# Kernel optimization log

Hardware: AMD Instinct MI355X
Metric: run time of the kernel (lower is better)

## Reference

```python
import jax, jax.numpy as jnp
import numpy as np

INPUT_DIM = 1024
EMBED_DIM = 1024
NUM_HEADS = 16
HEAD_DIM = EMBED_DIM // NUM_HEADS


def _xavier_uniform(key, shape):
    fan_in, fan_out = shape[1], shape[0]
    limit = float(np.sqrt(6.0 / (fan_in + fan_out)))
    return jax.random.uniform(key, shape, jnp.float32, -limit, limit)


def setup_inputs() -> dict:
    key = jax.random.key(0)
    kx, kqkv, ko = jax.random.split(key, 3)
    x = jax.random.normal(kx, (2, 2048, INPUT_DIM), jnp.float32)
    # torch Linear stores weight as [out, in]; we keep that convention
    w_qkv = _xavier_uniform(kqkv, (3 * EMBED_DIM, INPUT_DIM))
    b_qkv = jnp.zeros((3 * EMBED_DIM,), jnp.float32)
    w_o = _xavier_uniform(ko, (EMBED_DIM, EMBED_DIM))
    b_o = jnp.zeros((EMBED_DIM,), jnp.float32)
    return {"x": x, "w_qkv": w_qkv, "b_qkv": b_qkv, "w_o": w_o, "b_o": b_o}


def reference(x, w_qkv, b_qkv, w_o, b_o):
    B, S, _ = x.shape
    H, D = NUM_HEADS, HEAD_DIM
    qkv = jnp.einsum("bsi,oi->bso", x, w_qkv) + b_qkv          # [B,S,3E]
    qkv = qkv.reshape(B, S, H, 3 * D).transpose(0, 2, 1, 3)    # [B,H,S,3D]
    q, k, v = jnp.split(qkv, 3, axis=-1)                        # each [B,H,S,D]
    scores = jnp.einsum("bhqd,bhkd->bhqk", q, k) / jnp.sqrt(jnp.float32(D))
    attn = jax.nn.softmax(scores, axis=-1)                      # [B,H,S,S]
    vals = jnp.einsum("bhqk,bhkd->bhqd", attn, v)               # [B,H,S,D]
    vals = vals.transpose(0, 2, 1, 3).reshape(B, S, H * D)      # [B,S,E]
    return jnp.einsum("bse,oe->bso", vals, w_o) + b_o
```

## Files before the change

kernel.cpp:

```cpp
#include <hip/hip_runtime.h>
#include <hip/hip_bf16.h>


typedef __attribute__((ext_vector_type(8))) short bf16x8;
typedef __attribute__((ext_vector_type(4))) short bf16x4;
typedef __attribute__((ext_vector_type(4))) float f32x4;

#define MFMA16(a, b, c) __builtin_amdgcn_mfma_f32_16x16x32_bf16((a), (b), (c), 0, 0, 0)

#if __has_builtin(__builtin_amdgcn_exp2f)
#define EXP2F(x) __builtin_amdgcn_exp2f(x)
#else
#define EXP2F(x) exp2f(x)
#endif

static __device__ __forceinline__ unsigned short f2bf_bits(float v) {
    __hip_bfloat16 h = __float2bfloat16(v);
    return *reinterpret_cast<unsigned short*>(&h);
}

static __device__ __forceinline__ bf16x8 cvt8(const float* p) {
    const f32x4 a = reinterpret_cast<const f32x4*>(p)[0];
    const f32x4 b = reinterpret_cast<const f32x4*>(p)[1];
    bf16x8 r;
    r[0] = (short)f2bf_bits(a[0]); r[1] = (short)f2bf_bits(a[1]);
    r[2] = (short)f2bf_bits(a[2]); r[3] = (short)f2bf_bits(a[3]);
    r[4] = (short)f2bf_bits(b[0]); r[5] = (short)f2bf_bits(b[1]);
    r[6] = (short)f2bf_bits(b[2]); r[7] = (short)f2bf_bits(b[3]);
    return r;
}

__device__ __forceinline__ bf16x8 ldg8(const __hip_bfloat16* p) {
    return *reinterpret_cast<const bf16x8*>(p);
}

__device__ __forceinline__ void load16_lds(const __hip_bfloat16* g, unsigned short* l) {
    __builtin_amdgcn_global_load_lds(
        (const __attribute__((address_space(1))) void*)g,
        (__attribute__((address_space(3))) void*)l, 16, 0, 0);
}

__global__ __launch_bounds__(256)
void cast2_f32_bf16(const float* __restrict__ x, __hip_bfloat16* __restrict__ xb,
                    const float* __restrict__ w, __hip_bfloat16* __restrict__ wb) {
    const int bid = blockIdx.x;
    const float* src = (bid < 512) ? x : w;
    __hip_bfloat16* dst = (bid < 512) ? xb : wb;
    const int rb = (bid < 512) ? bid : (bid - 512);
    const size_t base = (size_t)rb * 8192 + (size_t)threadIdx.x * 32;
#pragma unroll
    for (int i = 0; i < 4; ++i)
        *reinterpret_cast<bf16x8*>(dst + base + i * 8) = cvt8(src + base + i * 8);
}

__global__ __launch_bounds__(256)
void cast_f32_bf16(const float* __restrict__ src, __hip_bfloat16* __restrict__ dst) {
    const size_t base = ((size_t)blockIdx.x * 256 + threadIdx.x) * 32;
#pragma unroll
    for (int i = 0; i < 4; ++i)
        *reinterpret_cast<bf16x8*>(dst + base + i * 8) = cvt8(src + base + i * 8);
}

__global__ __launch_bounds__(256)
void qkv_gemm(const __hip_bfloat16* __restrict__ xb,
              const __hip_bfloat16* __restrict__ wb,
              const float* __restrict__ bqkv,
              __hip_bfloat16* __restrict__ Q,
              __hip_bfloat16* __restrict__ K,
              __hip_bfloat16* __restrict__ Vt) {
    __shared__ unsigned short As[128 * 32];
    __shared__ unsigned short Bs[128 * 32];

    const int tid  = threadIdx.x;
    const int lane = tid & 63;
    const int wv   = tid >> 6;
    const int quad = lane >> 4;
    const int l16  = lane & 15;
    const int wm   = wv >> 1;
    const int wn   = wv & 1;

    const int bid = blockIdx.x;
    const int xcd = bid & 7;
    const int r   = bid >> 3;
    const int m0  = (r / 3) * 128;
    const int n0  = (xcd * 3 + (r % 3)) * 128;

    const __hip_bfloat16* agl = xb + (size_t)(m0 + wv * 32 + (lane >> 2)) * 1024 + (lane & 3) * 8;
    const __hip_bfloat16* bgl = wb + (size_t)(n0 + wv * 32 + (lane >> 2)) * 1024 + (lane & 3) * 8;
    unsigned short* al0 = &As[(wv * 32) * 32];
    unsigned short* al1 = &As[(wv * 32 + 16) * 32];
    unsigned short* bl0 = &Bs[(wv * 32) * 32];
    unsigned short* bl1 = &Bs[(wv * 32 + 16) * 32];

    f32x4 zv = {0.f, 0.f, 0.f, 0.f};
    f32x4 acc[4][4];
#pragma unroll
    for (int ii = 0; ii < 4; ++ii)
#pragma unroll
        for (int jj = 0; jj < 4; ++jj) acc[ii][jj] = zv;

    for (int k0 = 0; k0 < 1024; k0 += 32) {
        load16_lds(agl + k0, al0);
        load16_lds(agl + 16 * 1024 + k0, al1);
        load16_lds(bgl + k0, bl0);
        load16_lds(bgl + 16 * 1024 + k0, bl1);
        __syncthreads();
        bf16x8 af[4], bf[4];
#pragma unroll
        for (int ii = 0; ii < 4; ++ii)
            af[ii] = *reinterpret_cast<const bf16x8*>(
                &As[(wm * 64 + ii * 16 + l16) * 32 + quad * 8]);
#pragma unroll
        for (int jj = 0; jj < 4; ++jj)
            bf[jj] = *reinterpret_cast<const bf16x8*>(
                &Bs[(wn * 64 + jj * 16 + l16) * 32 + quad * 8]);
#pragma unroll
        for (int ii = 0; ii < 4; ++ii)
#pragma unroll
            for (int jj = 0; jj < 4; ++jj)
                acc[ii][jj] = MFMA16(af[ii], bf[jj], acc[ii][jj]);
        __syncthreads();
    }

    const float QSCALE = 0.18033688011f;

#pragma unroll
    for (int jj = 0; jj < 4; ++jj) {
        const int n = n0 + wn * 64 + jj * 16 + l16;
        const float bias = bqkv[n];
        const int h = n / 192;
        const int r2 = n - h * 192;
        const int t = r2 >> 6;
        const int d = r2 & 63;
#pragma unroll
        for (int ii = 0; ii < 4; ++ii) {
#pragma unroll
            for (int i = 0; i < 4; ++i) {
                const int m = m0 + wm * 64 + ii * 16 + quad * 4 + i;
                const int b = m >> 11;
                const int s = m & 2047;
                const int bh = b * 16 + h;
                float v = acc[ii][jj][i] + bias;
                if (t == 0) {
                    Q[((size_t)bh * 2048 + s) * 64 + d] = __float2bfloat16(v * QSCALE);
                } else if (t == 1) {
                    K[((size_t)bh * 2048 + s) * 64 + d] = __float2bfloat16(v);
                } else {
                    Vt[((size_t)bh * 64 + d) * 2048 + s] = __float2bfloat16(v);
                }
            }
        }
    }
}

__global__ __launch_bounds__(256)
void attn_kernel(const __hip_bfloat16* __restrict__ Q,
                 const __hip_bfloat16* __restrict__ K,
                 const __hip_bfloat16* __restrict__ Vt,
                 __hip_bfloat16* __restrict__ AO) {
    __shared__ unsigned short Ks0[32 * 40];
    __shared__ unsigned short Ks1[32 * 40];
    __shared__ unsigned short Vs[64 * 40];

    const int tid  = threadIdx.x;
    const int lane = tid & 63;
    const int wv   = tid >> 6;
    const int quad = lane >> 4;
    const int l16  = lane & 15;

    const int blk = blockIdx.x;
    const int xcd = blk & 7;
    const int sub = blk >> 3;
    const int bh  = xcd * 4 + (sub & 3);
    const int qb  = sub >> 2;
    const int q0  = qb * 128 + wv * 32;
    const int b   = bh >> 4;
    const int h   = bh & 15;

    const __hip_bfloat16* Qp = Q  + (size_t)bh * 131072;
    const __hip_bfloat16* Kp = K  + (size_t)bh * 131072;
    const __hip_bfloat16* Vp = Vt + (size_t)bh * 131072;

    bf16x8 bQ[2][2];
#pragma unroll
    for (int t = 0; t < 2; ++t)
#pragma unroll
        for (int dh = 0; dh < 2; ++dh)
            bQ[t][dh] = ldg8(Qp + (size_t)(q0 + t * 16 + l16) * 64 + dh * 32 + quad * 8);

    const int kr = tid >> 3;
    const int kc = (tid & 7) * 8;
    const int kb = kr & 7;
    const int sig = (kb < 4) ? ((kr >> 3) * 4 + kb) : (16 + (kr >> 3) * 4 + (kb - 4));
    unsigned short* kw = (kc < 32) ? &Ks0[sig * 40 + kc] : &Ks1[sig * 40 + (kc - 32)];
    const int vr = tid >> 2;
    const int vc = (tid & 3) * 8;
    unsigned short* vw = &Vs[vr * 40 + vc];

    f32x4 zv = {0.f, 0.f, 0.f, 0.f};
    f32x4 Of[2][4];
#pragma unroll
    for (int t = 0; t < 2; ++t)
#pragma unroll
        for (int jj = 0; jj < 4; ++jj) Of[t][jj] = zv;
    float li[2] = {0.f, 0.f};

    for (int kt = 0; kt < 64; ++kt) {
        const int key0 = kt * 32;

        const bf16x8 gk = ldg8(Kp + (size_t)(key0 + kr) * 64 + kc);
        const bf16x8 gv = ldg8(Vp + (size_t)vr * 2048 + key0 + vc);
        __syncthreads();
        *reinterpret_cast<bf16x8*>(kw) = gk;
        *reinterpret_cast<bf16x8*>(vw) = gv;
        __syncthreads();

        const bf16x8 aKA0 = *reinterpret_cast<const bf16x8*>(&Ks0[l16 * 40 + quad * 8]);
        const bf16x8 aKA1 = *reinterpret_cast<const bf16x8*>(&Ks1[l16 * 40 + quad * 8]);
        const bf16x8 aKB0 = *reinterpret_cast<const bf16x8*>(&Ks0[(16 + l16) * 40 + quad * 8]);
        const bf16x8 aKB1 = *reinterpret_cast<const bf16x8*>(&Ks1[(16 + l16) * 40 + quad * 8]);
        bf16x8 aV[4];
#pragma unroll
        for (int jj = 0; jj < 4; ++jj)
            aV[jj] = *reinterpret_cast<const bf16x8*>(&Vs[(jj * 16 + l16) * 40 + quad * 8]);

        f32x4 sA[2], sB[2];
#pragma unroll
        for (int t = 0; t < 2; ++t) {
            sA[t] = zv; sB[t] = zv;
            sA[t] = MFMA16(aKA0, bQ[t][0], sA[t]);
            sA[t] = MFMA16(aKA1, bQ[t][1], sA[t]);
            sB[t] = MFMA16(aKB0, bQ[t][0], sB[t]);
            sB[t] = MFMA16(aKB1, bQ[t][1], sB[t]);
        }

#pragma unroll
        for (int t = 0; t < 2; ++t) {
            float pA[4], pB[4];
#pragma unroll
            for (int i = 0; i < 4; ++i) {
                pA[i] = EXP2F(sA[t][i]);
                pB[i] = EXP2F(sB[t][i]);
            }
            li[t] += ((pA[0] + pA[1]) + (pA[2] + pA[3]))
                   + ((pB[0] + pB[1]) + (pB[2] + pB[3]));

            bf16x8 bP;
            bP[0] = (short)f2bf_bits(pA[0]); bP[1] = (short)f2bf_bits(pA[1]);
            bP[2] = (short)f2bf_bits(pA[2]); bP[3] = (short)f2bf_bits(pA[3]);
            bP[4] = (short)f2bf_bits(pB[0]); bP[5] = (short)f2bf_bits(pB[1]);
            bP[6] = (short)f2bf_bits(pB[2]); bP[7] = (short)f2bf_bits(pB[3]);

#pragma unroll
            for (int jj = 0; jj < 4; ++jj)
                Of[t][jj] = MFMA16(aV[jj], bP, Of[t][jj]);
        }
    }

#pragma unroll
    for (int t = 0; t < 2; ++t) {
        li[t] += __shfl_xor(li[t], 16);
        li[t] += __shfl_xor(li[t], 32);
    }

#pragma unroll
    for (int t = 0; t < 2; ++t) {
        const float linv = 1.f / li[t];
        const int s = q0 + t * 16 + l16;
        __hip_bfloat16* aop = AO + (((size_t)b * 2048 + s) * 16 + h) * 64;
#pragma unroll
        for (int jj = 0; jj < 4; ++jj) {
            bf16x4 pk;
#pragma unroll
            for (int i = 0; i < 4; ++i)
                pk[i] = (short)f2bf_bits(Of[t][jj][i] * linv);
            *reinterpret_cast<bf16x4*>(aop + jj * 16 + quad * 4) = pk;
        }
    }
}

__global__ __launch_bounds__(256)
void out_gemm(const __hip_bfloat16* __restrict__ A,
              const __hip_bfloat16* __restrict__ wob,
              const float* __restrict__ bo,
              float* __restrict__ out) {
    __shared__ unsigned short As[64 * 32];
    __shared__ unsigned short Bs[128 * 32];

    const int tid  = threadIdx.x;
    const int lane = tid & 63;
    const int wv   = tid >> 6;
    const int quad = lane >> 4;
    const int l16  = lane & 15;
    const int wm   = wv >> 1;
    const int wn   = wv & 1;

    const int bid = blockIdx.x;
    const int m0  = (bid >> 3) * 64;
    const int n0  = (bid & 7) * 128;

    const __hip_bfloat16* agl = A   + (size_t)(m0 + wv * 16 + (lane >> 2)) * 1024 + (lane & 3) * 8;
    const __hip_bfloat16* bgl = wob + (size_t)(n0 + wv * 32 + (lane >> 2)) * 1024 + (lane & 3) * 8;
    unsigned short* al0 = &As[(wv * 16) * 32];
    unsigned short* bl0 = &Bs[(wv * 32) * 32];
    unsigned short* bl1 = &Bs[(wv * 32 + 16) * 32];

    f32x4 zv = {0.f, 0.f, 0.f, 0.f};
    f32x4 acc[2][4];
#pragma unroll
    for (int ii = 0; ii < 2; ++ii)
#pragma unroll
        for (int jj = 0; jj < 4; ++jj) acc[ii][jj] = zv;

    for (int k0 = 0; k0 < 1024; k0 += 32) {
        load16_lds(agl + k0, al0);
        load16_lds(bgl + k0, bl0);
        load16_lds(bgl + 16 * 1024 + k0, bl1);
        __syncthreads();
        bf16x8 af[2], bf[4];
#pragma unroll
        for (int ii = 0; ii < 2; ++ii)
            af[ii] = *reinterpret_cast<const bf16x8*>(
                &As[(wm * 32 + ii * 16 + l16) * 32 + quad * 8]);
#pragma unroll
        for (int jj = 0; jj < 4; ++jj)
            bf[jj] = *reinterpret_cast<const bf16x8*>(
                &Bs[(wn * 64 + jj * 16 + l16) * 32 + quad * 8]);
#pragma unroll
        for (int ii = 0; ii < 2; ++ii)
#pragma unroll
            for (int jj = 0; jj < 4; ++jj)
                acc[ii][jj] = MFMA16(af[ii], bf[jj], acc[ii][jj]);
        __syncthreads();
    }

#pragma unroll
    for (int jj = 0; jj < 4; ++jj) {
        const int n = n0 + wn * 64 + jj * 16 + l16;
        const float bias = bo[n];
#pragma unroll
        for (int ii = 0; ii < 2; ++ii) {
#pragma unroll
            for (int i = 0; i < 4; ++i) {
                const int m = m0 + wm * 32 + ii * 16 + quad * 4 + i;
                out[(size_t)m * 1024 + n] = acc[ii][jj][i] + bias;
            }
        }
    }
}

extern "C" void kernel_launch(void* const* d_in, const int* in_sizes, int n_in,
                              void* d_out, int out_size, void* d_ws, size_t ws_size,
                              hipStream_t stream) {
    const float* x    = (const float*)d_in[0];
    const float* wqkv = (const float*)d_in[1];
    const float* bqkv = (const float*)d_in[2];
    const float* wo   = (const float*)d_in[3];
    const float* bo   = (const float*)d_in[4];
    float* out = (float*)d_out;

    __hip_bfloat16* ws = (__hip_bfloat16*)d_ws;
    __hip_bfloat16* Q   = ws;
    __hip_bfloat16* K   = ws + (size_t)4194304;
    __hip_bfloat16* Vt  = ws + (size_t)8388608;
    __hip_bfloat16* AO  = ws + (size_t)12582912;
    __hip_bfloat16* wob = Q;

    __hip_bfloat16* xb     = (__hip_bfloat16*)d_out;
    __hip_bfloat16* wqkvb  = xb + (size_t)4194304;

    cast2_f32_bf16<<<dim3(896), 256, 0, stream>>>(x, xb, wqkv, wqkvb);
    qkv_gemm<<<dim3(768), 256, 0, stream>>>(xb, wqkvb, bqkv, Q, K, Vt);
    attn_kernel<<<dim3(512), 256, 0, stream>>>(Q, K, Vt, AO);
    cast_f32_bf16<<<dim3(128), 256, 0, stream>>>(wo, wob);
    out_gemm<<<dim3(512), 256, 0, stream>>>(AO, wob, bo, out);
}
```

Before: 203.2 us.

## Double-buffer LDS tiles in GEMMs and attention, vectorize V-transpose stores

Adds ping-pong shared-memory buffers to the QKV GEMM, the attention kernel and the output GEMM, so the next K-tile's global loads are issued before the current tile's MFMAs. The aim is to hide global-memory latency and cut one barrier per iteration. The QKV epilogue also writes the transposed V as packed 4-element bf16 vectors instead of scalar stores. In exchange it doubles LDS use per block, which may lower occupancy. The GEMM loops rely on the barrier kept at the end of each iteration to avoid races on the buffer being overwritten.

```diff
diff --git a/kernel.cpp b/kernel.cpp
--- a/kernel.cpp
+++ b/kernel.cpp
@@ -68,8 +68,8 @@
               __hip_bfloat16* __restrict__ Q,
               __hip_bfloat16* __restrict__ K,
               __hip_bfloat16* __restrict__ Vt) {
-    __shared__ unsigned short As[128 * 32];
-    __shared__ unsigned short Bs[128 * 32];
+    __shared__ unsigned short As[2][128 * 32];
+    __shared__ unsigned short Bs[2][128 * 32];
 
     const int tid  = threadIdx.x;
     const int lane = tid & 63;
@@ -87,10 +87,6 @@
 
     const __hip_bfloat16* agl = xb + (size_t)(m0 + wv * 32 + (lane >> 2)) * 1024 + (lane & 3) * 8;
     const __hip_bfloat16* bgl = wb + (size_t)(n0 + wv * 32 + (lane >> 2)) * 1024 + (lane & 3) * 8;
-    unsigned short* al0 = &As[(wv * 32) * 32];
-    unsigned short* al1 = &As[(wv * 32 + 16) * 32];
-    unsigned short* bl0 = &Bs[(wv * 32) * 32];
-    unsigned short* bl1 = &Bs[(wv * 32 + 16) * 32];
 
     f32x4 zv = {0.f, 0.f, 0.f, 0.f};
     f32x4 acc[4][4];
@@ -99,21 +95,30 @@
 #pragma unroll
         for (int jj = 0; jj < 4; ++jj) acc[ii][jj] = zv;
 
+    load16_lds(agl, &As[0][(wv * 32) * 32]);
+    load16_lds(agl + 16 * 1024, &As[0][(wv * 32 + 16) * 32]);
+    load16_lds(bgl, &Bs[0][(wv * 32) * 32]);
+    load16_lds(bgl + 16 * 1024, &Bs[0][(wv * 32 + 16) * 32]);
+    __syncthreads();
+
     for (int k0 = 0; k0 < 1024; k0 += 32) {
-        load16_lds(agl + k0, al0);
-        load16_lds(agl + 16 * 1024 + k0, al1);
-        load16_lds(bgl + k0, bl0);
-        load16_lds(bgl + 16 * 1024 + k0, bl1);
-        __syncthreads();
+        const int p = (k0 >> 5) & 1;
+        if (k0 + 32 < 1024) {
+            const int q = p ^ 1;
+            load16_lds(agl + k0 + 32, &As[q][(wv * 32) * 32]);
+            load16_lds(agl + 16 * 1024 + k0 + 32, &As[q][(wv * 32 + 16) * 32]);
+            load16_lds(bgl + k0 + 32, &Bs[q][(wv * 32) * 32]);
+            load16_lds(bgl + 16 * 1024 + k0 + 32, &Bs[q][(wv * 32 + 16) * 32]);
+        }
         bf16x8 af[4], bf[4];
 #pragma unroll
         for (int ii = 0; ii < 4; ++ii)
             af[ii] = *reinterpret_cast<const bf16x8*>(
-                &As[(wm * 64 + ii * 16 + l16) * 32 + quad * 8]);
+                &As[p][(wm * 64 + ii * 16 + l16) * 32 + quad * 8]);
 #pragma unroll
         for (int jj = 0; jj < 4; ++jj)
             bf[jj] = *reinterpret_cast<const bf16x8*>(
-                &Bs[(wn * 64 + jj * 16 + l16) * 32 + quad * 8]);
+                &Bs[p][(wn * 64 + jj * 16 + l16) * 32 + quad * 8]);
 #pragma unroll
         for (int ii = 0; ii < 4; ++ii)
 #pragma unroll
@@ -134,19 +139,24 @@
         const int d = r2 & 63;
 #pragma unroll
         for (int ii = 0; ii < 4; ++ii) {
-#pragma unroll
-            for (int i = 0; i < 4; ++i) {
-                const int m = m0 + wm * 64 + ii * 16 + quad * 4 + i;
-                const int b = m >> 11;
-                const int s = m & 2047;
-                const int bh = b * 16 + h;
-                float v = acc[ii][jj][i] + bias;
-                if (t == 0) {
-                    Q[((size_t)bh * 2048 + s) * 64 + d] = __float2bfloat16(v * QSCALE);
-                } else if (t == 1) {
-                    K[((size_t)bh * 2048 + s) * 64 + d] = __float2bfloat16(v);
-                } else {
-                    Vt[((size_t)bh * 64 + d) * 2048 + s] = __float2bfloat16(v);
+            const int mb = m0 + wm * 64 + ii * 16 + quad * 4;
+            const int b = mb >> 11;
+            const int s0 = mb & 2047;
+            const int bh = b * 16 + h;
+            if (t == 2) {
+                bf16x4 pk;
+#pragma unroll
+                for (int i = 0; i < 4; ++i)
+                    pk[i] = (short)f2bf_bits(acc[ii][jj][i] + bias);
+                *reinterpret_cast<bf16x4*>(&Vt[((size_t)bh * 64 + d) * 2048 + s0]) = pk;
+            } else {
+#pragma unroll
+                for (int i = 0; i < 4; ++i) {
+                    const float v = acc[ii][jj][i] + bias;
+                    if (t == 0)
+                        Q[((size_t)bh * 2048 + s0 + i) * 64 + d] = __float2bfloat16(v * QSCALE);
+                    else
+                        K[((size_t)bh * 2048 + s0 + i) * 64 + d] = __float2bfloat16(v);
                 }
             }
         }
@@ -158,9 +168,9 @@
                  const __hip_bfloat16* __restrict__ K,
                  const __hip_bfloat16* __restrict__ Vt,
                  __hip_bfloat16* __restrict__ AO) {
-    __shared__ unsigned short Ks0[32 * 40];
-    __shared__ unsigned short Ks1[32 * 40];
-    __shared__ unsigned short Vs[64 * 40];
+    __shared__ unsigned short Ks0[2][32 * 40];
+    __shared__ unsigned short Ks1[2][32 * 40];
+    __shared__ unsigned short Vs[2][64 * 40];
 
     const int tid  = threadIdx.x;
     const int lane = tid & 63;
@@ -192,10 +202,14 @@
     const int kc = (tid & 7) * 8;
     const int kb = kr & 7;
     const int sig = (kb < 4) ? ((kr >> 3) * 4 + kb) : (16 + (kr >> 3) * 4 + (kb - 4));
-    unsigned short* kw = (kc < 32) ? &Ks0[sig * 40 + kc] : &Ks1[sig * 40 + (kc - 32)];
+    const int koff = (kc < 32) ? (sig * 40 + kc) : (sig * 40 + (kc - 32));
+    const int kis1 = (kc >= 32);
     const int vr = tid >> 2;
     const int vc = (tid & 3) * 8;
-    unsigned short* vw = &Vs[vr * 40 + vc];
+    const int voff = vr * 40 + vc;
+
+    const __hip_bfloat16* kgp = Kp + (size_t)kr * 64 + kc;
+    const __hip_bfloat16* vgp = Vp + (size_t)vr * 2048 + vc;
 
     f32x4 zv = {0.f, 0.f, 0.f, 0.f};
     f32x4 Of[2][4];
@@ -205,24 +219,37 @@
         for (int jj = 0; jj < 4; ++jj) Of[t][jj] = zv;
     float li[2] = {0.f, 0.f};
 
+    bf16x8 gk = ldg8(kgp);
+    bf16x8 gv = ldg8(vgp);
+    {
+        unsigned short* kw0 = kis1 ? &Ks1[0][koff] : &Ks0[0][koff];
+        *reinterpret_cast<bf16x8*>(kw0) = gk;
+        *reinterpret_cast<bf16x8*>(&Vs[0][voff]) = gv;
+    }
+    gk = ldg8(kgp + (size_t)32 * 64);
+    gv = ldg8(vgp + 32);
+    __syncthreads();
+
     for (int kt = 0; kt < 64; ++kt) {
-        const int key0 = kt * 32;
-
-        const bf16x8 gk = ldg8(Kp + (size_t)(key0 + kr) * 64 + kc);
-        const bf16x8 gv = ldg8(Vp + (size_t)vr * 2048 + key0 + vc);
-        __syncthreads();
-        *reinterpret_cast<bf16x8*>(kw) = gk;
-        *reinterpret_cast<bf16x8*>(vw) = gv;
-        __syncthreads();
-
-        const bf16x8 aKA0 = *reinterpret_cast<const bf16x8*>(&Ks0[l16 * 40 + quad * 8]);
-        const bf16x8 aKA1 = *reinterpret_cast<const bf16x8*>(&Ks1[l16 * 40 + quad * 8]);
-        const bf16x8 aKB0 = *reinterpret_cast<const bf16x8*>(&Ks0[(16 + l16) * 40 + quad * 8]);
-        const bf16x8 aKB1 = *reinterpret_cast<const bf16x8*>(&Ks1[(16 + l16) * 40 + quad * 8]);
+        const int p = kt & 1;
+        if (kt < 63) {
+            unsigned short* kw1 = kis1 ? &Ks1[p ^ 1][koff] : &Ks0[p ^ 1][koff];
+            *reinterpret_cast<bf16x8*>(kw1) = gk;
+            *reinterpret_cast<bf16x8*>(&Vs[p ^ 1][voff]) = gv;
+        }
+        if (kt < 62) {
+            gk = ldg8(kgp + (size_t)(kt + 2) * 32 * 64);
+            gv = ldg8(vgp + (kt + 2) * 32);
+        }
+
+        const bf16x8 aKA0 = *reinterpret_cast<const bf16x8*>(&Ks0[p][l16 * 40 + quad * 8]);
+        const bf16x8 aKA1 = *reinterpret_cast<const bf16x8*>(&Ks1[p][l16 * 40 + quad * 8]);
+        const bf16x8 aKB0 = *reinterpret_cast<const bf16x8*>(&Ks0[p][(16 + l16) * 40 + quad * 8]);
+        const bf16x8 aKB1 = *reinterpret_cast<const bf16x8*>(&Ks1[p][(16 + l16) * 40 + quad * 8]);
         bf16x8 aV[4];
 #pragma unroll
         for (int jj = 0; jj < 4; ++jj)
-            aV[jj] = *reinterpret_cast<const bf16x8*>(&Vs[(jj * 16 + l16) * 40 + quad * 8]);
+            aV[jj] = *reinterpret_cast<const bf16x8*>(&Vs[p][(jj * 16 + l16) * 40 + quad * 8]);
 
         f32x4 sA[2], sB[2];
 #pragma unroll
@@ -255,6 +282,7 @@
             for (int jj = 0; jj < 4; ++jj)
                 Of[t][jj] = MFMA16(aV[jj], bP, Of[t][jj]);
         }
+        __syncthreads();
     }
 
 #pragma unroll
@@ -284,8 +312,8 @@
               const __hip_bfloat16* __restrict__ wob,
               const float* __restrict__ bo,
               float* __restrict__ out) {
-    __shared__ unsigned short As[64 * 32];
-    __shared__ unsigned short Bs[128 * 32];
+    __shared__ unsigned short As[2][64 * 32];
+    __shared__ unsigned short Bs[2][128 * 32];
 
     const int tid  = threadIdx.x;
     const int lane = tid & 63;
@@ -301,9 +329,6 @@
 
     const __hip_bfloat16* agl = A   + (size_t)(m0 + wv * 16 + (lane >> 2)) * 1024 + (lane & 3) * 8;
     const __hip_bfloat16* bgl = wob + (size_t)(n0 + wv * 32 + (lane >> 2)) * 1024 + (lane & 3) * 8;
-    unsigned short* al0 = &As[(wv * 16) * 32];
-    unsigned short* bl0 = &Bs[(wv * 32) * 32];
-    unsigned short* bl1 = &Bs[(wv * 32 + 16) * 32];
 
     f32x4 zv = {0.f, 0.f, 0.f, 0.f};
     f32x4 acc[2][4];
@@ -312,20 +337,28 @@
 #pragma unroll
         for (int jj = 0; jj < 4; ++jj) acc[ii][jj] = zv;
 
+    load16_lds(agl, &As[0][(wv * 16) * 32]);
+    load16_lds(bgl, &Bs[0][(wv * 32) * 32]);
+    load16_lds(bgl + 16 * 1024, &Bs[0][(wv * 32 + 16) * 32]);
+    __syncthreads();
+
     for (int k0 = 0; k0 < 1024; k0 += 32) {
-        load16_lds(agl + k0, al0);
-        load16_lds(bgl + k0, bl0);
-        load16_lds(bgl + 16 * 1024 + k0, bl1);
-        __syncthreads();
+        const int p = (k0 >> 5) & 1;
+        if (k0 + 32 < 1024) {
+            const int q = p ^ 1;
+            load16_lds(agl + k0 + 32, &As[q][(wv * 16) * 32]);
+            load16_lds(bgl + k0 + 32, &Bs[q][(wv * 32) * 32]);
+            load16_lds(bgl + 16 * 1024 + k0 + 32, &Bs[q][(wv * 32 + 16) * 32]);
+        }
         bf16x8 af[2], bf[4];
 #pragma unroll
         for (int ii = 0; ii < 2; ++ii)
             af[ii] = *reinterpret_cast<const bf16x8*>(
-                &As[(wm * 32 + ii * 16 + l16) * 32 + quad * 8]);
+                &As[p][(wm * 32 + ii * 16 + l16) * 32 + quad * 8]);
 #pragma unroll
         for (int jj = 0; jj < 4; ++jj)
             bf[jj] = *reinterpret_cast<const bf16x8*>(
-                &Bs[(wn * 64 + jj * 16 + l16) * 32 + quad * 8]);
+                &Bs[p][(wn * 64 + jj * 16 + l16) * 32 + quad * 8]);
 #pragma unroll
         for (int ii = 0; ii < 2; ++ii)
 #pragma unroll
```

Result: no change. 200.6 us (-1.3%).
